# Optimization experiments

Hardware: AMD Instinct MI355X
Metric: run time of the kernel (lower is better)

Reference implementation:

```python
import jax, jax.numpy as jnp
import numpy as np

H = 32          # query heads
KVH = 8         # kv heads (GQA)
D = 128         # head dim
GROUP = 128     # quantization group size along K
THETA = 10000.0 # RoPE base


def dequant_fp4(codes, scales):
    """FP4 E2M1-style dequant: w = (code - 8) * 0.5 * per-group scale.
    codes: [K, N] int32 in [0,16); scales: [K//GROUP, N] float32."""
    K, N = codes.shape
    g = K // GROUP
    w = (codes.astype(jnp.float32) - 8.0) * 0.5
    return (w.reshape(g, GROUP, N) * scales[:, None, :]).reshape(K, N)


def apply_rope(x, pos):
    """x: [B, S, h, D]; rotate-half RoPE."""
    half = D // 2
    inv_freq = 1.0 / (THETA ** (jnp.arange(half, dtype=jnp.float32) / half))
    ang = pos.astype(jnp.float32)[:, None] * inv_freq[None, :]  # [S, half]
    cos = jnp.cos(ang)[None, :, None, :]
    sin = jnp.sin(ang)[None, :, None, :]
    x1, x2 = x[..., :half], x[..., half:]
    return jnp.concatenate([x1 * cos - x2 * sin, x2 * cos + x1 * sin], axis=-1)


def setup_inputs() -> dict:
    key = jax.random.key(0)
    ks = jax.random.split(key, 9)
    B, S, HID = 1, 2048, H * D
    KV = KVH * D
    x = jax.random.normal(ks[0], (B, S, HID), dtype=jnp.float32)
    q_codes = jax.random.randint(ks[1], (HID, HID), 0, 16, dtype=jnp.int32)
    k_codes = jax.random.randint(ks[2], (HID, KV), 0, 16, dtype=jnp.int32)
    v_codes = jax.random.randint(ks[3], (HID, KV), 0, 16, dtype=jnp.int32)
    o_codes = jax.random.randint(ks[4], (HID, HID), 0, 16, dtype=jnp.int32)
    g = HID // GROUP
    mk = lambda k, n: jax.random.uniform(k, (g, n), dtype=jnp.float32) * 0.02 + 1e-3
    q_scales = mk(ks[5], HID)
    k_scales = mk(ks[6], KV)
    v_scales = mk(ks[7], KV)
    o_scales = mk(ks[8], HID)
    return {"x": x, "q_codes": q_codes, "k_codes": k_codes, "v_codes": v_codes,
            "o_codes": o_codes, "q_scales": q_scales, "k_scales": k_scales,
            "v_scales": v_scales, "o_scales": o_scales}


def reference(x, q_codes, k_codes, v_codes, o_codes,
              q_scales, k_scales, v_scales, o_scales):
    B, S, _ = x.shape
    Wq = dequant_fp4(q_codes, q_scales)  # [HID, HID]
    Wk = dequant_fp4(k_codes, k_scales)  # [HID, KVH*D]
    Wv = dequant_fp4(v_codes, v_scales)
    Wo = dequant_fp4(o_codes, o_scales)

    q = (x @ Wq).reshape(B, S, H, D)
    k = (x @ Wk).reshape(B, S, KVH, D)
    v = (x @ Wv).reshape(B, S, KVH, D)

    pos = jnp.arange(S)
    q = apply_rope(q, pos)
    k = apply_rope(k, pos)

    # GQA: expand kv heads to query heads (this is what reading the shared
    # KV cache per query-head group computes)
    rep = H // KVH
    k = jnp.repeat(k, rep, axis=2)  # [B, S, H, D]
    v = jnp.repeat(v, rep, axis=2)

    scale = 1.0 / jnp.sqrt(jnp.float32(D))
    scores = jnp.einsum('bqhd,bkhd->bhqk', q, k) * scale  # [B, H, S, S]
    causal = jnp.tril(jnp.ones((S, S), dtype=bool))
    scores = jnp.where(causal[None, None], scores, jnp.float32(-1e30))
    probs = jax.nn.softmax(scores, axis=-1)
    attn = jnp.einsum('bhqk,bkhd->bqhd', probs, v).reshape(B, S, H * D)
    return attn @ Wo
```

## Files before the change

kernel.cpp:

```cpp
#include <hip/hip_runtime.h>

typedef unsigned short u16;
typedef __attribute__((ext_vector_type(4))) float f32x4;
typedef __attribute__((ext_vector_type(4))) unsigned short u16x4;
typedef __attribute__((ext_vector_type(8))) short bf16x8;

#define S_LEN 2048
#define NH 32
#define NKVH 8
#define DHEAD 128
#define HID 4096
#define KVW 1024
#define QKVW 6144

__device__ __forceinline__ u16 f2bf(float f) {
  unsigned u = __float_as_uint(f);
  u = u + 0x7fffu + ((u >> 16) & 1u);
  return (u16)(u >> 16);
}
__device__ __forceinline__ float bf2f(u16 h) {
  return __uint_as_float(((unsigned)h) << 16);
}
__device__ __forceinline__ void async16(void* lds, const void* g) {
  __builtin_amdgcn_global_load_lds((const __attribute__((address_space(1))) void*)g,
                                   (__attribute__((address_space(3))) void*)lds, 16, 0, 0);
}
__device__ __forceinline__ f32x4 mfma16(bf16x8 a, bf16x8 b, f32x4 c) {
  return __builtin_amdgcn_mfma_f32_16x16x32_bf16(a, b, c, 0, 0, 0);
}
__device__ __forceinline__ unsigned cvtpk(float a, float b) {
  unsigned r;
  asm("v_cvt_pk_bf16_f32 %0, %1, %2" : "=v"(r) : "v"(a), "v"(b));
  return r;
}

__global__ __launch_bounds__(256) void f2bf4_kernel(const float* __restrict__ in,
                                                    u16* __restrict__ out) {
  size_t i = ((size_t)blockIdx.x * 256 + threadIdx.x) * 4;
  f32x4 v = *(const f32x4*)(in + i);
  u16x4 o;
  o.x = f2bf(v.x); o.y = f2bf(v.y); o.z = f2bf(v.z); o.w = f2bf(v.w);
  *(u16x4*)(out + i) = o;
}

__global__ __launch_bounds__(256) void dequant_t_kernel(const int* __restrict__ codes,
                                                        const float* __restrict__ scales,
                                                        u16* __restrict__ Wt,
                                                        int K, int N) {
  __shared__ float tile[32][33];
  const int tx = threadIdx.x & 31, ty = threadIdx.x >> 5;
  const int k0 = blockIdx.x * 32, n0 = blockIdx.y * 32;
  const float sc = scales[(size_t)(k0 >> 7) * N + n0 + tx];
#pragma unroll
  for (int i = 0; i < 4; ++i) {
    int k = k0 + ty + i * 8;
    int c = codes[(size_t)k * N + n0 + tx];
    tile[ty + i * 8][tx] = ((float)c - 8.0f) * 0.5f * sc;
  }
  __syncthreads();
#pragma unroll
  for (int i = 0; i < 4; ++i) {
    int n = n0 + ty + i * 8;
    Wt[(size_t)n * K + k0 + tx] = f2bf(tile[tx][ty + i * 8]);
  }
}

template <int NI, int OUTF32>
__global__ __launch_bounds__(512, 2) void gemm_w(const u16* __restrict__ A, int lda,
                                                 const u16* __restrict__ Bt, int ldb,
                                                 void* __restrict__ Cv, int ldc, int K) {
  constexpr int BN = NI * 32;
  constexpr int NB = NI / 2;
  constexpr int BSLOT = BN * 128;
  extern __shared__ char lds[];
  char* Bbase = lds + 65536;
  const int tid = threadIdx.x, w = tid >> 6, lane = tid & 63;
  const int lo = lane & 15, hi = lane >> 4;
  const int wm = w >> 1, wn = w & 1;
  const int id = blockIdx.x;
  const int g = id & 7, r = id >> 3;
  const int bm = r >> 2, bn = g * 4 + (r & 3);
  const int m0 = bm * 256, n0 = bn * BN;

  const int srow = tid >> 3, schunk = (tid & 7) ^ (srow & 7);
  const char* Ab = (const char*)(A + (size_t)(m0 + srow) * lda) + schunk * 16;
  const char* Bb = (const char*)(Bt + (size_t)(n0 + srow) * ldb) + schunk * 16;

  f32x4 acc[4][NI];
#pragma unroll
  for (int i = 0; i < 4; ++i)
#pragma unroll
    for (int j = 0; j < NI; ++j) acc[i][j] = (f32x4){0.f, 0.f, 0.f, 0.f};

  auto stageA = [&](int buf, int k1) {
#pragma unroll
    for (int u = 0; u < 2; ++u) {
      char* dst = lds + buf * 32768 + u * 8192 + w * 1024;
      async16(dst, Ab + ((size_t)(u * 64) * lda + k1) * 2);
      async16(dst + 16384, Ab + ((size_t)(u * 64 + 128) * lda + k1) * 2);
    }
  };
  auto stageB = [&](int slot, int k1) {
#pragma unroll
    for (int j = 0; j < NB; ++j)
      async16(Bbase + slot * BSLOT + j * 8192 + w * 1024,
              Bb + ((size_t)(j * 64) * ldb + k1) * 2);
  };

  const int xm = (lo & 7) << 4;
  const int aro = (wm >> 1) * 16384 + (wm & 1) * 8192 + lo * 128;
  int bofs[NI];
#pragma unroll
  for (int ni = 0; ni < NI; ++ni) {
    int n = wn * (NI * 16) + ni * 16 + lo;
    bofs[ni] = (n >> 6) * 8192 + (n & 63) * 128;
  }

  auto ldfrags = [&](const char* As, const char* Bs, int kk, bf16x8* Afo, bf16x8* Bfo) {
    const int ck = (kk * 64 + hi * 16) ^ xm;
#pragma unroll
    for (int i = 0; i < 4; ++i) Afo[i] = *(const bf16x8*)(As + aro + i * 2048 + ck);
#pragma unroll
    for (int ni = 0; ni < NI; ++ni) Bfo[ni] = *(const bf16x8*)(Bs + bofs[ni] + ck);
  };

  stageA(0, 0);
  stageB(0, 0);
  stageB(1, 64);
  asm volatile("s_waitcnt vmcnt(%0)" ::"i"(NB) : "memory");
  __builtin_amdgcn_s_barrier();

  bf16x8 Afc[4], Bfc[NI], Afn[4], Bfn[NI];
  ldfrags(lds, Bbase, 0, Afc, Bfc);

  const int KT = K >> 6;
  int ab = 0, bb = 0;
  for (int t = 0; t < KT; ++t) {
    const char* As = lds + ab * 32768;
    const char* Bs = Bbase + bb * BSLOT;
    const bool m1 = t + 1 < KT, m2 = t + 2 < KT;
    int bs2 = bb + 2; if (bs2 >= 3) bs2 -= 3;
    int bn1 = bb + 1; if (bn1 >= 3) bn1 -= 3;
    if (m1) stageA(ab ^ 1, (t + 1) << 6);
    ldfrags(As, Bs, 1, Afn, Bfn);
    __builtin_amdgcn_sched_barrier(0);
    __builtin_amdgcn_s_setprio(1);
#pragma unroll
    for (int i = 0; i < 4; ++i)
#pragma unroll
      for (int ni = 0; ni < NI; ++ni)
        acc[i][ni] = mfma16(Afc[i], Bfc[ni], acc[i][ni]);
    __builtin_amdgcn_s_setprio(0);
    if (m2) stageB(bs2, (t + 2) << 6);
    __builtin_amdgcn_s_setprio(1);
#pragma unroll
    for (int i = 0; i < 4; ++i)
#pragma unroll
      for (int ni = 0; ni < NI; ++ni)
        acc[i][ni] = mfma16(Afn[i], Bfn[ni], acc[i][ni]);
    __builtin_amdgcn_s_setprio(0);
    if (m1) {
      if (m2) asm volatile("s_waitcnt vmcnt(%0)" ::"i"(NB) : "memory");
      else    asm volatile("s_waitcnt vmcnt(0)" ::: "memory");
      __builtin_amdgcn_s_barrier();
      ldfrags(lds + (ab ^ 1) * 32768, Bbase + bn1 * BSLOT, 0, Afc, Bfc);
      __builtin_amdgcn_sched_barrier(0);
    }
    ab ^= 1;
    if (++bb == 3) bb = 0;
  }
#pragma unroll
  for (int mi = 0; mi < 4; ++mi)
#pragma unroll
    for (int ni = 0; ni < NI; ++ni) {
      size_t row = (size_t)(m0 + wm * 64 + mi * 16 + hi * 4);
      size_t col = (size_t)(n0 + wn * (NI * 16) + ni * 16 + lo);
#pragma unroll
      for (int rr = 0; rr < 4; ++rr) {
        size_t idx = (row + rr) * ldc + col;
        if (OUTF32) ((float*)Cv)[idx] = acc[mi][ni][rr];
        else ((u16*)Cv)[idx] = f2bf(acc[mi][ni][rr]);
      }
    }
}

__global__ void rope_tab_kernel(float* __restrict__ ctab, float* __restrict__ stab) {
  int s = blockIdx.x, d = threadIdx.x;
  float inv = exp2f(-(float)d * 0.2076205059304601f);
  float ang = (float)s * inv;
  ctab[s * 64 + d] = cosf(ang);
  stab[s * 64 + d] = sinf(ang);
}

__global__ __launch_bounds__(256) void rope_kernel(u16* __restrict__ qkv,
                                                   const float* __restrict__ ctab,
                                                   const float* __restrict__ stab) {
  int s = blockIdx.x;
  int head = blockIdx.y * 4 + (threadIdx.x >> 6);
  int d = threadIdx.x & 63;
  int col = head < NH ? head * DHEAD + d : HID + (head - NH) * DHEAD + d;
  size_t base = (size_t)s * QKVW + col;
  float c = ctab[s * 64 + d], sn = stab[s * 64 + d];
  float x1 = bf2f(qkv[base]);
  float x2 = bf2f(qkv[base + 64]);
  qkv[base] = f2bf(x1 * c - x2 * sn);
  qkv[base + 64] = f2bf(x2 * c + x1 * sn);
}

__global__ __launch_bounds__(256) void vtrans_kernel(const u16* __restrict__ qkv,
                                                     u16* __restrict__ Vt) {
  __shared__ u16 tile[32][33];
  const int tx = threadIdx.x & 31, ty = threadIdx.x >> 5;
  const int s0 = blockIdx.x * 32, c0 = blockIdx.y * 32;
#pragma unroll
  for (int i = 0; i < 4; ++i)
    tile[ty + i * 8][tx] = qkv[(size_t)(s0 + ty + i * 8) * QKVW + (HID + KVW) + c0 + tx];
  __syncthreads();
#pragma unroll
  for (int i = 0; i < 4; ++i)
    Vt[(size_t)(c0 + ty + i * 8) * S_LEN + s0 + tx] = tile[tx][ty + i * 8];
}

__global__ __launch_bounds__(256, 4) void attn_kernel(const u16* __restrict__ qkv,
                                                      const u16* __restrict__ Vt,
                                                      u16* __restrict__ attnO) {
  __shared__ alignas(16) u16 Ks[64 * 128];
  __shared__ alignas(16) u16 Vs[128 * 64];
  __shared__ alignas(16) unsigned Ps32[4][16][32];
  const int tid = threadIdx.x, w = tid >> 6, lane = tid & 63;
  const int lo = lane & 15, hi = lane >> 4;
  const unsigned pxor = (unsigned)((lo & 7) << 2);
  const int bx = blockIdx.x, h = blockIdx.y, kvh = h >> 2;
  const u16* Kbase = qkv + HID + kvh * DHEAD;
  const u16* Vbase = Vt + (size_t)kvh * DHEAD * S_LEN;
  const int krow = w * 4 + hi;
  const int kscn = lo;
  const int vrow = w * 8 + (lane >> 3);
  const int vscn = lane & 7;

#pragma unroll 1
  for (int pass = 0; pass < 2; ++pass) {
    const int qb = pass == 0 ? (31 - bx) : bx;
    const int qrow0 = qb * 64 + w * 16;
    bf16x8 qf[4];
    {
      const u16* qp = qkv + (size_t)(qrow0 + lo) * QKVW + h * DHEAD;
      const float qs = 0.08838834764831845f * 1.4426950408889634f;
#pragma unroll
      for (int dc = 0; dc < 4; ++dc) {
        bf16x8 v = *(const bf16x8*)(qp + dc * 32 + hi * 8);
#pragma unroll
        for (int j = 0; j < 8; ++j) v[j] = (short)f2bf(bf2f((u16)v[j]) * qs);
        qf[dc] = v;
      }
    }
    f32x4 oacc[8];
#pragma unroll
    for (int i = 0; i < 8; ++i) oacc[i] = (f32x4){0.f, 0.f, 0.f, 0.f};
    float m_run = -1e30f, l_run = 0.f;

    const int nt = qb + 1;
    for (int kt = 0; kt < nt; ++kt) {
#pragma unroll
      for (int i = 0; i < 4; ++i) {
        int kr = i * 16 + krow;
        async16((char*)&Ks[0] + (i * 16 + w * 4) * 256,
                (const char*)(Kbase + (size_t)(kt * 64 + kr) * QKVW + (kscn ^ (kr & 7)) * 8));
        int vr = i * 32 + vrow;
        async16((char*)&Vs[0] + (i * 32 + w * 8) * 128,
                (const char*)(Vbase + (size_t)vr * S_LEN + kt * 64 + (vscn ^ (vr & 7)) * 8));
      }
      __syncthreads();
      f32x4 st[4];
#pragma unroll
      for (int t = 0; t < 4; ++t) st[t] = (f32x4){0.f, 0.f, 0.f, 0.f};
#pragma unroll
      for (int t = 0; t < 4; ++t) {
        int kq = t * 16 + lo;
#pragma unroll
        for (int dc = 0; dc < 4; ++dc) {
          bf16x8 kf = *(const bf16x8*)((const char*)&Ks[0] + kq * 256 +
                                       (((dc << 2) + hi) ^ (kq & 7)) * 16);
          st[t] = mfma16(kf, qf[dc], st[t]);
        }
      }
      if (kt == qb) {
#pragma unroll
        for (int t = 0; t < 4; ++t)
#pragma unroll
          for (int r = 0; r < 4; ++r) {
            int kposl = t * 16 + 4 * hi + r;
            st[t][r] = (kposl <= w * 16 + lo) ? st[t][r] : -1e30f;
          }
      }
      float mloc = st[0][0];
#pragma unroll
      for (int t = 0; t < 4; ++t)
#pragma unroll
        for (int r = 0; r < 4; ++r) mloc = fmaxf(mloc, st[t][r]);
      mloc = fmaxf(mloc, __shfl_xor(mloc, 16, 64));
      mloc = fmaxf(mloc, __shfl_xor(mloc, 32, 64));
      if (!__all(mloc - m_run <= 8.0f)) {
        float mn = fmaxf(m_run, mloc);
        float alpha = exp2f(m_run - mn);
        m_run = mn;
        l_run *= alpha;
#pragma unroll
        for (int dt = 0; dt < 8; ++dt)
#pragma unroll
          for (int r = 0; r < 4; ++r) oacc[dt][r] *= alpha;
      }
      float psum = 0.f;
#pragma unroll
      for (int t = 0; t < 4; ++t)
#pragma unroll
        for (int r = 0; r < 4; ++r) {
          float p = exp2f(st[t][r] - m_run);
          st[t][r] = p;
          psum += p;
        }
      psum += __shfl_xor(psum, 16, 64);
      psum += __shfl_xor(psum, 32, 64);
      l_run += psum;
#pragma unroll
      for (int t = 0; t < 4; ++t)
#pragma unroll
        for (int rp = 0; rp < 2; ++rp)
          Ps32[w][lo][(unsigned)(8 * t + 2 * hi + rp) ^ pxor] =
              cvtpk(st[t][2 * rp], st[t][2 * rp + 1]);
      bf16x8 pf[2];
#pragma unroll
      for (int kc = 0; kc < 2; ++kc)
        pf[kc] = *(const bf16x8*)&Ps32[w][lo][(unsigned)(kc * 16 + hi * 4) ^ pxor];
#pragma unroll
      for (int dt = 0; dt < 8; ++dt) {
        int d = dt * 16 + lo;
#pragma unroll
        for (int kc = 0; kc < 2; ++kc) {
          bf16x8 vf = *(const bf16x8*)((const char*)&Vs[0] + d * 128 +
                                       (((kc << 2) + hi) ^ (d & 7)) * 16);
          oacc[dt] = mfma16(vf, pf[kc], oacc[dt]);
        }
      }
      __syncthreads();
    }
    float linv = 1.0f / l_run;
    u16* op = attnO + (size_t)(qrow0 + lo) * HID + h * DHEAD;
#pragma unroll
    for (int dt = 0; dt < 8; ++dt) {
      u16x4 o4;
#pragma unroll
      for (int r = 0; r < 4; ++r) o4[r] = f2bf(oacc[dt][r] * linv);
      *(u16x4*)(op + dt * 16 + 4 * hi) = o4;
    }
  }
}

extern "C" void kernel_launch(void* const* d_in, const int* in_sizes, int n_in,
                              void* d_out, int out_size, void* d_ws, size_t ws_size,
                              hipStream_t stream) {
  const float* x = (const float*)d_in[0];
  const int* qc = (const int*)d_in[1];
  const int* kc = (const int*)d_in[2];
  const int* vc = (const int*)d_in[3];
  const int* oc = (const int*)d_in[4];
  const float* qs = (const float*)d_in[5];
  const float* ks = (const float*)d_in[6];
  const float* vs = (const float*)d_in[7];
  const float* os = (const float*)d_in[8];
  float* out = (float*)d_out;
  char* ws = (char*)d_ws;

  u16* xb    = (u16*)(ws);
  u16* qkv   = (u16*)(ws + 16777216);
  u16* attnb = (u16*)(ws + 41943040);
  u16* Vt    = (u16*)(ws + 58720256);
  u16* Wbig  = (u16*)(ws + 62914560);
  float* ctab = (float*)Vt;
  float* stab = (float*)(ws + 58720256 + 524288);

  f2bf4_kernel<<<8192, 256, 0, stream>>>(x, xb);
  dequant_t_kernel<<<dim3(128, 128), 256, 0, stream>>>(qc, qs, Wbig, HID, HID);
  dequant_t_kernel<<<dim3(128, 32), 256, 0, stream>>>(kc, ks, Wbig + (size_t)HID * HID, HID, KVW);
  dequant_t_kernel<<<dim3(128, 32), 256, 0, stream>>>(vc, vs, Wbig + (size_t)(HID + KVW) * HID, HID, KVW);
  rope_tab_kernel<<<2048, 64, 0, stream>>>(ctab, stab);
  gemm_w<6, 0><<<256, 512, 139264, stream>>>(xb, HID, Wbig, HID, qkv, QKVW, HID);
  rope_kernel<<<dim3(S_LEN, (NH + NKVH) / 4), 256, 0, stream>>>(qkv, ctab, stab);
  vtrans_kernel<<<dim3(64, 32), 256, 0, stream>>>(qkv, Vt);
  attn_kernel<<<dim3(16, 32), 256, 0, stream>>>(qkv, Vt, attnb);
  dequant_t_kernel<<<dim3(128, 128), 256, 0, stream>>>(oc, os, Wbig, HID, HID);
  gemm_w<4, 1><<<256, 512, 114688, stream>>>(attnb, HID, Wbig, HID, out, HID, HID);
}
```

Before: 318.2 us.

## Split attention into one q-block per workgroup with KV-head-grouped block ordering

The attention kernel no longer has each workgroup process a paired long and short q-block in two passes. It now launches 1024 workgroups, each handling a single 64-row q-block. The block index is remapped so that the eight KV-head groups are interleaved across adjacent blocks. The four query heads sharing a KV head sit close together for K/V cache reuse, and q-blocks are issued in a heavy/light alternating order for load balance. The intent is more parallelism and better L2 locality, at the risk of per-workgroup tail imbalance and extra Q-load and setup overhead.

```diff
diff --git a/kernel.cpp b/kernel.cpp
--- a/kernel.cpp
+++ b/kernel.cpp
@@ -230,7 +230,13 @@
   const int tid = threadIdx.x, w = tid >> 6, lane = tid & 63;
   const int lo = lane & 15, hi = lane >> 4;
   const unsigned pxor = (unsigned)((lo & 7) << 2);
-  const int bx = blockIdx.x, h = blockIdx.y, kvh = h >> 2;
+  const int id = blockIdx.x;
+  const int g = id & 7, r = id >> 3;
+  const int hd = g * 4 + (r & 3);
+  const int rq = r >> 2;
+  const int a = rq & 7, b = rq >> 3;
+  const int qb = (b & 1) ? (31 - a - 8 * (b >> 1)) : (a + 8 * (b >> 1));
+  const int kvh = g;
   const u16* Kbase = qkv + HID + kvh * DHEAD;
   const u16* Vbase = Vt + (size_t)kvh * DHEAD * S_LEN;
   const int krow = w * 4 + hi;
@@ -238,121 +244,117 @@
   const int vrow = w * 8 + (lane >> 3);
   const int vscn = lane & 7;
 
-#pragma unroll 1
-  for (int pass = 0; pass < 2; ++pass) {
-    const int qb = pass == 0 ? (31 - bx) : bx;
-    const int qrow0 = qb * 64 + w * 16;
-    bf16x8 qf[4];
-    {
-      const u16* qp = qkv + (size_t)(qrow0 + lo) * QKVW + h * DHEAD;
-      const float qs = 0.08838834764831845f * 1.4426950408889634f;
+  const int qrow0 = qb * 64 + w * 16;
+  bf16x8 qf[4];
+  {
+    const u16* qp = qkv + (size_t)(qrow0 + lo) * QKVW + hd * DHEAD;
+    const float qs = 0.08838834764831845f * 1.4426950408889634f;
+#pragma unroll
+    for (int dc = 0; dc < 4; ++dc) {
+      bf16x8 v = *(const bf16x8*)(qp + dc * 32 + hi * 8);
+#pragma unroll
+      for (int j = 0; j < 8; ++j) v[j] = (short)f2bf(bf2f((u16)v[j]) * qs);
+      qf[dc] = v;
+    }
+  }
+  f32x4 oacc[8];
+#pragma unroll
+  for (int i = 0; i < 8; ++i) oacc[i] = (f32x4){0.f, 0.f, 0.f, 0.f};
+  float m_run = -1e30f, l_run = 0.f;
+
+  const int nt = qb + 1;
+  for (int kt = 0; kt < nt; ++kt) {
+#pragma unroll
+    for (int i = 0; i < 4; ++i) {
+      int kr = i * 16 + krow;
+      async16((char*)&Ks[0] + (i * 16 + w * 4) * 256,
+              (const char*)(Kbase + (size_t)(kt * 64 + kr) * QKVW + (kscn ^ (kr & 7)) * 8));
+      int vr = i * 32 + vrow;
+      async16((char*)&Vs[0] + (i * 32 + w * 8) * 128,
+              (const char*)(Vbase + (size_t)vr * S_LEN + kt * 64 + (vscn ^ (vr & 7)) * 8));
+    }
+    __syncthreads();
+    f32x4 st[4];
+#pragma unroll
+    for (int t = 0; t < 4; ++t) st[t] = (f32x4){0.f, 0.f, 0.f, 0.f};
+#pragma unroll
+    for (int t = 0; t < 4; ++t) {
+      int kq = t * 16 + lo;
 #pragma unroll
       for (int dc = 0; dc < 4; ++dc) {
-        bf16x8 v = *(const bf16x8*)(qp + dc * 32 + hi * 8);
-#pragma unroll
-        for (int j = 0; j < 8; ++j) v[j] = (short)f2bf(bf2f((u16)v[j]) * qs);
-        qf[dc] = v;
+        bf16x8 kf = *(const bf16x8*)((const char*)&Ks[0] + kq * 256 +
+                                     (((dc << 2) + hi) ^ (kq & 7)) * 16);
+        st[t] = mfma16(kf, qf[dc], st[t]);
       }
     }
-    f32x4 oacc[8];
-#pragma unroll
-    for (int i = 0; i < 8; ++i) oacc[i] = (f32x4){0.f, 0.f, 0.f, 0.f};
-    float m_run = -1e30f, l_run = 0.f;
-
-    const int nt = qb + 1;
-    for (int kt = 0; kt < nt; ++kt) {
-#pragma unroll
-      for (int i = 0; i < 4; ++i) {
-        int kr = i * 16 + krow;
-        async16((char*)&Ks[0] + (i * 16 + w * 4) * 256,
-                (const char*)(Kbase + (size_t)(kt * 64 + kr) * QKVW + (kscn ^ (kr & 7)) * 8));
-        int vr = i * 32 + vrow;
-        async16((char*)&Vs[0] + (i * 32 + w * 8) * 128,
-                (const char*)(Vbase + (size_t)vr * S_LEN + kt * 64 + (vscn ^ (vr & 7)) * 8));
+    if (kt == qb) {
+#pragma unroll
+      for (int t = 0; t < 4; ++t)
+#pragma unroll
+        for (int r2 = 0; r2 < 4; ++r2) {
+          int kposl = t * 16 + 4 * hi + r2;
+          st[t][r2] = (kposl <= w * 16 + lo) ? st[t][r2] : -1e30f;
+        }
+    }
+    float mloc = st[0][0];
+#pragma unroll
+    for (int t = 0; t < 4; ++t)
+#pragma unroll
+      for (int r2 = 0; r2 < 4; ++r2) mloc = fmaxf(mloc, st[t][r2]);
+    mloc = fmaxf(mloc, __shfl_xor(mloc, 16, 64));
+    mloc = fmaxf(mloc, __shfl_xor(mloc, 32, 64));
+    if (!__all(mloc - m_run <= 8.0f)) {
+      float mn = fmaxf(m_run, mloc);
+      float alpha = exp2f(m_run - mn);
+      m_run = mn;
+      l_run *= alpha;
+#pragma unroll
+      for (int dt = 0; dt < 8; ++dt)
+#pragma unroll
+        for (int r2 = 0; r2 < 4; ++r2) oacc[dt][r2] *= alpha;
+    }
+    float psum = 0.f;
+#pragma unroll
+    for (int t = 0; t < 4; ++t)
+#pragma unroll
+      for (int r2 = 0; r2 < 4; ++r2) {
+        float p = exp2f(st[t][r2] - m_run);
+        st[t][r2] = p;
+        psum += p;
       }
-      __syncthreads();
-      f32x4 st[4];
-#pragma unroll
-      for (int t = 0; t < 4; ++t) st[t] = (f32x4){0.f, 0.f, 0.f, 0.f};
-#pragma unroll
-      for (int t = 0; t < 4; ++t) {
-        int kq = t * 16 + lo;
-#pragma unroll
-        for (int dc = 0; dc < 4; ++dc) {
-          bf16x8 kf = *(const bf16x8*)((const char*)&Ks[0] + kq * 256 +
-                                       (((dc << 2) + hi) ^ (kq & 7)) * 16);
-          st[t] = mfma16(kf, qf[dc], st[t]);
-        }
+    psum += __shfl_xor(psum, 16, 64);
+    psum += __shfl_xor(psum, 32, 64);
+    l_run += psum;
+#pragma unroll
+    for (int t = 0; t < 4; ++t)
+#pragma unroll
+      for (int rp = 0; rp < 2; ++rp)
+        Ps32[w][lo][(unsigned)(8 * t + 2 * hi + rp) ^ pxor] =
+            cvtpk(st[t][2 * rp], st[t][2 * rp + 1]);
+    bf16x8 pf[2];
+#pragma unroll
+    for (int kc = 0; kc < 2; ++kc)
+      pf[kc] = *(const bf16x8*)&Ps32[w][lo][(unsigned)(kc * 16 + hi * 4) ^ pxor];
+#pragma unroll
+    for (int dt = 0; dt < 8; ++dt) {
+      int d = dt * 16 + lo;
+#pragma unroll
+      for (int kc = 0; kc < 2; ++kc) {
+        bf16x8 vf = *(const bf16x8*)((const char*)&Vs[0] + d * 128 +
+                                     (((kc << 2) + hi) ^ (d & 7)) * 16);
+        oacc[dt] = mfma16(vf, pf[kc], oacc[dt]);
       }
-      if (kt == qb) {
-#pragma unroll
-        for (int t = 0; t < 4; ++t)
-#pragma unroll
-          for (int r = 0; r < 4; ++r) {
-            int kposl = t * 16 + 4 * hi + r;
-            st[t][r] = (kposl <= w * 16 + lo) ? st[t][r] : -1e30f;
-          }
-      }
-      float mloc = st[0][0];
-#pragma unroll
-      for (int t = 0; t < 4; ++t)
-#pragma unroll
-        for (int r = 0; r < 4; ++r) mloc = fmaxf(mloc, st[t][r]);
-      mloc = fmaxf(mloc, __shfl_xor(mloc, 16, 64));
-      mloc = fmaxf(mloc, __shfl_xor(mloc, 32, 64));
-      if (!__all(mloc - m_run <= 8.0f)) {
-        float mn = fmaxf(m_run, mloc);
-        float alpha = exp2f(m_run - mn);
-        m_run = mn;
-        l_run *= alpha;
-#pragma unroll
-        for (int dt = 0; dt < 8; ++dt)
-#pragma unroll
-          for (int r = 0; r < 4; ++r) oacc[dt][r] *= alpha;
-      }
-      float psum = 0.f;
-#pragma unroll
-      for (int t = 0; t < 4; ++t)
-#pragma unroll
-        for (int r = 0; r < 4; ++r) {
-          float p = exp2f(st[t][r] - m_run);
-          st[t][r] = p;
-          psum += p;
-        }
-      psum += __shfl_xor(psum, 16, 64);
-      psum += __shfl_xor(psum, 32, 64);
-      l_run += psum;
-#pragma unroll
-      for (int t = 0; t < 4; ++t)
-#pragma unroll
-        for (int rp = 0; rp < 2; ++rp)
-          Ps32[w][lo][(unsigned)(8 * t + 2 * hi + rp) ^ pxor] =
-              cvtpk(st[t][2 * rp], st[t][2 * rp + 1]);
-      bf16x8 pf[2];
-#pragma unroll
-      for (int kc = 0; kc < 2; ++kc)
-        pf[kc] = *(const bf16x8*)&Ps32[w][lo][(unsigned)(kc * 16 + hi * 4) ^ pxor];
-#pragma unroll
-      for (int dt = 0; dt < 8; ++dt) {
-        int d = dt * 16 + lo;
-#pragma unroll
-        for (int kc = 0; kc < 2; ++kc) {
-          bf16x8 vf = *(const bf16x8*)((const char*)&Vs[0] + d * 128 +
-                                       (((kc << 2) + hi) ^ (d & 7)) * 16);
-          oacc[dt] = mfma16(vf, pf[kc], oacc[dt]);
-        }
-      }
-      __syncthreads();
-    }
-    float linv = 1.0f / l_run;
-    u16* op = attnO + (size_t)(qrow0 + lo) * HID + h * DHEAD;
-#pragma unroll
-    for (int dt = 0; dt < 8; ++dt) {
-      u16x4 o4;
-#pragma unroll
-      for (int r = 0; r < 4; ++r) o4[r] = f2bf(oacc[dt][r] * linv);
-      *(u16x4*)(op + dt * 16 + 4 * hi) = o4;
-    }
+    }
+    __syncthreads();
+  }
+  float linv = 1.0f / l_run;
+  u16* op = attnO + (size_t)(qrow0 + lo) * HID + hd * DHEAD;
+#pragma unroll
+  for (int dt = 0; dt < 8; ++dt) {
+    u16x4 o4;
+#pragma unroll
+    for (int r2 = 0; r2 < 4; ++r2) o4[r2] = f2bf(oacc[dt][r2] * linv);
+    *(u16x4*)(op + dt * 16 + 4 * hi) = o4;
   }
 }
 
@@ -387,7 +389,7 @@
   gemm_w<6, 0><<<256, 512, 139264, stream>>>(xb, HID, Wbig, HID, qkv, QKVW, HID);
   rope_kernel<<<dim3(S_LEN, (NH + NKVH) / 4), 256, 0, stream>>>(qkv, ctab, stab);
   vtrans_kernel<<<dim3(64, 32), 256, 0, stream>>>(qkv, Vt);
-  attn_kernel<<<dim3(16, 32), 256, 0, stream>>>(qkv, Vt, attnb);
+  attn_kernel<<<1024, 256, 0, stream>>>(qkv, Vt, attnb);
   dequant_t_kernel<<<dim3(128, 128), 256, 0, stream>>>(oc, os, Wbig, HID, HID);
   gemm_w<4, 1><<<256, 512, 114688, stream>>>(attnb, HID, Wbig, HID, out, HID, HID);
 }
```

Measured after the change: 321.3 us. Within noise of the previous version (+1.0%).
